# Kernel optimization log

Hardware: AMD Instinct MI355X
Metric: run time of the kernel (lower is better)

The kernel has to match this reference:

```python
import jax, jax.numpy as jnp
import numpy as np

B, H, S, D = 2, 8, 4096, 64
TEMPERATURE = 8.0


def setup_inputs() -> dict:
    key = jax.random.key(0)
    kq, kk, kv, km = jax.random.split(key, 4)
    q = jax.random.normal(kq, (B, H, S, D), dtype=jnp.float32)
    k = jax.random.normal(kk, (B, H, S, D), dtype=jnp.float32)
    v = jax.random.normal(kv, (B, H, S, D), dtype=jnp.float32)
    mask = jax.random.randint(km, (1, 1, S, S), 0, 2, dtype=jnp.int32)
    return {"q": q, "k": k, "v": v, "mask": mask}


def reference(q, k, v, mask):
    # scores = q @ k^T / temperature  -> [B,H,S,S]
    scores = jnp.einsum("bhqd,bhkd->bhqk", q, k) / TEMPERATURE
    # masked_fill(mask == 0, -inf)
    scores = jnp.where(mask == 0, -jnp.inf, scores)
    attn = jax.nn.softmax(scores, axis=-1)
    output = jnp.einsum("bhqk,bhkd->bhqd", attn, v)
    return (output, attn)
```

## Files before the change

### kernel.cpp

```cpp
#include <hip/hip_runtime.h>
#include <stdint.h>

typedef __attribute__((ext_vector_type(8))) short short8;
typedef __attribute__((ext_vector_type(4))) float float4v;

#define SEQ 4096
#define HD 64
#define QB 128
#define KT 64
#define HEADS 16
#define NT (SEQ / KT)
#define MWORDS (SEQ / 64)
#define TILE_BYTES 8192
#define QSCALE 0.18033688f

__device__ __forceinline__ ushort f2bf(float f) {
    union { float f; uint32_t u; } x; x.f = f;
    uint32_t u = x.u;
    return (ushort)((u + 0x7FFFu + ((u >> 16) & 1u)) >> 16);
}

__device__ __forceinline__ uint32_t cvt_pk_bf16(float lo, float hi) {
    uint32_t r;
    asm("v_cvt_pk_bf16_f32 %0, %1, %2" : "=v"(r) : "v"(lo), "v"(hi));
    return r;
}

__device__ __forceinline__ float exp2_hw(float x) { return __builtin_amdgcn_exp2f(x); }
__device__ __forceinline__ float log2_hw(float x) { return __builtin_amdgcn_logf(x); }

__device__ __forceinline__ void gload_lds16(const void* g, void* l) {
    __builtin_amdgcn_global_load_lds(
        (const __attribute__((address_space(1))) uint32_t*)g,
        (__attribute__((address_space(3))) uint32_t*)l, 16, 0, 0);
}

__global__ __launch_bounds__(256) void pack_mask_kernel(const int* __restrict__ mask,
                                                        unsigned long long* __restrict__ mb) {
    const int qrow = blockIdx.x;
    const int wave = threadIdx.x >> 6;
    const int lane = threadIdx.x & 63;
    const int* rp = mask + (size_t)qrow * SEQ;
    #pragma unroll
    for (int i = 0; i < 16; ++i) {
        const int widx = wave * 16 + i;
        const int mv = rp[widx * 64 + lane];
        unsigned long long b = __ballot(mv != 0);
        if (lane == 0) mb[(size_t)qrow * MWORDS + widx] = b;
    }
}

__global__ __launch_bounds__(256) void prep_kv_kernel(const float* __restrict__ kg,
                                                      const float* __restrict__ vg,
                                                      char* __restrict__ ktiles,
                                                      char* __restrict__ vtiles) {
    __shared__ __align__(16) float Tl[64][68];
    const int bid = blockIdx.x;
    const int tid = threadIdx.x;
    const float* Kg = kg + (size_t)bid * KT * HD;
    const float* Vg = vg + (size_t)bid * KT * HD;
    char* Kt = ktiles + (size_t)bid * TILE_BYTES;
    char* Vt = vtiles + (size_t)bid * TILE_BYTES;

    {
        const int r = tid >> 2, c0 = (tid & 3) * 16;
        #pragma unroll
        for (int j = 0; j < 4; ++j)
            *(float4v*)&Tl[r][c0 + j * 4] = *(const float4v*)(Kg + r * HD + c0 + j * 4);
    }
    __syncthreads();
    #pragma unroll
    for (int cc = 0; cc < 2; ++cc) {
        const int c = tid + cc * 256;
        const int t = c >> 7, h = (c >> 6) & 1, g = (c >> 4) & 3, li = c & 15;
        const int row = 32 * (t >> 1) + 8 * (li >> 2) + 4 * (t & 1) + (li & 3);
        const float* src = &Tl[row][h * 32 + g * 8];
        short8 w;
        #pragma unroll
        for (int e = 0; e < 8; ++e) w[e] = (short)f2bf(src[e]);
        *(short8*)(Kt + c * 16) = w;
    }
    __syncthreads();
    {
        const int r = tid >> 2, c0 = (tid & 3) * 16;
        #pragma unroll
        for (int j = 0; j < 4; ++j)
            *(float4v*)&Tl[r][c0 + j * 4] = *(const float4v*)(Vg + r * HD + c0 + j * 4);
    }
    __syncthreads();
    #pragma unroll
    for (int cc = 0; cc < 2; ++cc) {
        const int c = tid + cc * 256;
        const int dt = c >> 7, h = (c >> 6) & 1, g = (c >> 4) & 3, li = c & 15;
        short8 w;
        #pragma unroll
        for (int e = 0; e < 8; ++e) w[e] = (short)f2bf(Tl[h * 32 + g * 8 + e][dt * 16 + li]);
        *(short8*)(Vt + c * 16) = w;
    }
}

#define STAGE_K8(KTI, DST) do {                                                    \
    const char* _s = Ktile + (size_t)(KTI) * TILE_BYTES + wave * 1024 + lane * 16; \
    gload_lds16(_s, (char*)(DST) + wave * 1024);                                   \
} while (0)

#define STAGE2_K(KTI) do {                                                              \
    const char* _s = Ktile + (size_t)(KTI) * TILE_BYTES + ew * 2048 + lane * 16;        \
    char* _d = (char*)LdsK[(KTI) & 3] + ew * 2048;                                      \
    gload_lds16(_s, _d); gload_lds16(_s + 1024, _d + 1024);                             \
} while (0)

#define STAGE2_V(KTI) do {                                                              \
    const char* _s = Vtile + (size_t)(KTI) * TILE_BYTES + ew * 2048 + lane * 16;        \
    char* _d = (char*)LdsV[(KTI) & 3] + ew * 2048;                                      \
    gload_lds16(_s, _d); gload_lds16(_s + 1024, _d + 1024);                             \
} while (0)

__global__ __launch_bounds__(512, 4) void attn_kernel(
    const float* __restrict__ qg, const unsigned long long* __restrict__ mb,
    const char* __restrict__ ktiles, const char* __restrict__ vtiles,
    float* __restrict__ outg, float* __restrict__ attng)
{
    __shared__ __align__(16) char LdsK[4][TILE_BYTES];
    __shared__ __align__(16) char LdsV[4][TILE_BYTES];

    const int tid  = threadIdx.x;
    const int wave = tid >> 6;
    const int lane = tid & 63;
    const int g    = lane >> 4;
    const int li   = lane & 15;

    const int bid = blockIdx.x;
    const int blk = (bid & 7) * 64 + (bid >> 3);
    const int bh  = blk >> 5;
    const int qb  = blk & 31;

    const size_t qkvBase = (size_t)bh * SEQ * HD;
    const float* Qg = qg + qkvBase + (size_t)qb * QB * HD;
    const char* Ktile = ktiles + (size_t)bh * NT * TILE_BYTES;
    const char* Vtile = vtiles + (size_t)bh * NT * TILE_BYTES;

    const int wq0 = wave * 16;
    short8 aq[2];
    #pragma unroll
    for (int h = 0; h < 2; ++h) {
        const float* src = Qg + (wq0 + li) * HD + h * 32 + g * 8;
        short8 t;
        #pragma unroll
        for (int e = 0; e < 8; ++e) t[e] = (short)f2bf(src[e] * QSCALE);
        aq[h] = t;
    }

    const int qrow = qb * QB + wq0 + li;
    const unsigned long long* mrow = mb + (size_t)qrow * MWORDS;

    STAGE_K8(0, LdsK[0]);
    STAGE_K8(1, LdsK[1]);
    asm volatile("s_waitcnt vmcnt(1)" ::: "memory");
    __builtin_amdgcn_s_barrier();
    asm volatile("" ::: "memory");

    float lsum = 0.f;
    for (int kt = 0; kt < NT; ++kt) {
        if (kt + 2 < NT) STAGE_K8(kt + 2, LdsK[(kt + 2) % 3]);
        const unsigned long long mw = mrow[kt];
        const uint32_t mlo = (uint32_t)mw >> (g * 8);
        const uint32_t mhi = (uint32_t)(mw >> 32) >> (g * 8);

        const char* Kb = LdsK[kt % 3] + lane * 16;
        short8 bk[4][2];
        #pragma unroll
        for (int t = 0; t < 4; ++t)
            #pragma unroll
            for (int h = 0; h < 2; ++h)
                bk[t][h] = *(const short8*)(Kb + (t * 2 + h) * 1024);

        float4v accs[4];
        #pragma unroll
        for (int t = 0; t < 4; ++t) accs[t] = (float4v){0.f, 0.f, 0.f, 0.f};
        __builtin_amdgcn_s_setprio(1);
        #pragma unroll
        for (int t = 0; t < 4; ++t) {
            accs[t] = __builtin_amdgcn_mfma_f32_16x16x32_bf16(bk[t][0], aq[0], accs[t], 0, 0, 0);
            accs[t] = __builtin_amdgcn_mfma_f32_16x16x32_bf16(bk[t][1], aq[1], accs[t], 0, 0, 0);
        }
        __builtin_amdgcn_s_setprio(0);
        const uint32_t nib[4] = { mlo & 0xFu, (mlo >> 4) & 0xFu, mhi & 0xFu, (mhi >> 4) & 0xFu };
        #pragma unroll
        for (int t = 0; t < 4; ++t) {
            #pragma unroll
            for (int r = 0; r < 4; ++r) {
                const float e = exp2_hw(accs[t][r]);
                lsum += ((nib[t] >> r) & 1u) ? e : 0.f;
            }
        }
        if (kt < NT - 2) {
            asm volatile("s_waitcnt vmcnt(2)" ::: "memory");
            __builtin_amdgcn_s_barrier();
            asm volatile("" ::: "memory");
        } else if (kt == NT - 2) {
            asm volatile("s_waitcnt vmcnt(1)" ::: "memory");
            __builtin_amdgcn_s_barrier();
            asm volatile("" ::: "memory");
        }
    }
    lsum += __shfl_xor(lsum, 16);
    lsum += __shfl_xor(lsum, 32);
    const float linv2 = -log2_hw(lsum);

    float* attnT = attng + (size_t)bh * SEQ * SEQ + (size_t)qrow * SEQ + g * 8;
    float4v acco[4];
    #pragma unroll
    for (int dt = 0; dt < 4; ++dt) acco[dt] = (float4v){0.f, 0.f, 0.f, 0.f};

    const int odd = wave & 1;
    const int ew  = wave >> 1;

    __syncthreads();
    unsigned long long mwreg = mrow[0];
    if (!odd) {
        STAGE2_K(0); STAGE2_V(0);
        STAGE2_K(1); STAGE2_V(1);
        asm volatile("s_waitcnt vmcnt(0)" ::: "memory");
    }
    __builtin_amdgcn_s_barrier();
    asm volatile("" ::: "memory");

    float4v accs[4];
    for (int slot = 0; slot < 2 * NT + 1; ++slot) {
        const int half = slot & 1;
        int t_qk = -1, t_fin = -1;
        if (!odd) {
            if (!half) { const int t = slot >> 1; if (t < NT) t_qk = t; }
            else       t_fin = slot >> 1;
        } else {
            if (half)  t_qk = slot >> 1;
            else if (slot > 0) t_fin = (slot >> 1) - 1;
        }

        if (t_qk >= 0) {
            if (!odd && t_qk + 2 < NT) { STAGE2_K(t_qk + 2); STAGE2_V(t_qk + 2); }
            const char* Kb = LdsK[t_qk & 3] + lane * 16;
            short8 bk[4][2];
            #pragma unroll
            for (int t = 0; t < 4; ++t)
                #pragma unroll
                for (int h = 0; h < 2; ++h)
                    bk[t][h] = *(const short8*)(Kb + (t * 2 + h) * 1024);
            #pragma unroll
            for (int t = 0; t < 4; ++t) accs[t] = (float4v){0.f, 0.f, 0.f, 0.f};
            __builtin_amdgcn_s_setprio(1);
            #pragma unroll
            for (int t = 0; t < 4; ++t) {
                accs[t] = __builtin_amdgcn_mfma_f32_16x16x32_bf16(bk[t][0], aq[0], accs[t], 0, 0, 0);
                accs[t] = __builtin_amdgcn_mfma_f32_16x16x32_bf16(bk[t][1], aq[1], accs[t], 0, 0, 0);
            }
            __builtin_amdgcn_s_setprio(0);
        }

        if (t_fin >= 0) {
            const char* Vb = LdsV[t_fin & 3] + lane * 16;
            short8 vb[4][2];
            #pragma unroll
            for (int t = 0; t < 4; ++t)
                #pragma unroll
                for (int h = 0; h < 2; ++h)
                    vb[t][h] = *(const short8*)(Vb + (t * 2 + h) * 1024);

            const uint32_t mlo = (uint32_t)mwreg >> (g * 8);
            const uint32_t mhi = (uint32_t)(mwreg >> 32) >> (g * 8);
            const uint32_t nib[4] = { mlo & 0xFu, (mlo >> 4) & 0xFu, mhi & 0xFu, (mhi >> 4) & 0xFu };
            float4v pv[4];
            #pragma unroll
            for (int t = 0; t < 4; ++t)
                #pragma unroll
                for (int r = 0; r < 4; ++r) {
                    const float e = exp2_hw(accs[t][r] + linv2);
                    pv[t][r] = ((nib[t] >> r) & 1u) ? e : 0.f;
                }

            float* ap = attnT + t_fin * KT;
            *(float4v*)(ap)      = pv[0];
            *(float4v*)(ap + 4)  = pv[1];
            *(float4v*)(ap + 32) = pv[2];
            *(float4v*)(ap + 36) = pv[3];

            if (t_fin + 1 < NT) mwreg = mrow[t_fin + 1];

            uint32_t pk[4][2];
            #pragma unroll
            for (int t = 0; t < 4; ++t) {
                pk[t][0] = cvt_pk_bf16(pv[t][0], pv[t][1]);
                pk[t][1] = cvt_pk_bf16(pv[t][2], pv[t][3]);
            }
            union { uint32_t u[4]; short8 s; } pa0, pa1;
            pa0.u[0] = pk[0][0]; pa0.u[1] = pk[0][1]; pa0.u[2] = pk[1][0]; pa0.u[3] = pk[1][1];
            pa1.u[0] = pk[2][0]; pa1.u[1] = pk[2][1]; pa1.u[2] = pk[3][0]; pa1.u[3] = pk[3][1];

            __builtin_amdgcn_s_setprio(1);
            #pragma unroll
            for (int dt = 0; dt < 4; ++dt) {
                acco[dt] = __builtin_amdgcn_mfma_f32_16x16x32_bf16(vb[dt][0], pa0.s, acco[dt], 0, 0, 0);
                acco[dt] = __builtin_amdgcn_mfma_f32_16x16x32_bf16(vb[dt][1], pa1.s, acco[dt], 0, 0, 0);
            }
            __builtin_amdgcn_s_setprio(0);
        }

        if (slot < 2 * NT) {
            if (t_qk >= 0 || t_fin >= 0)
                asm volatile("s_waitcnt vmcnt(5)" ::: "memory");
            __builtin_amdgcn_s_barrier();
            asm volatile("" ::: "memory");
        }
    }

    float* outW = outg + qkvBase + (size_t)qrow * HD + g * 4;
    #pragma unroll
    for (int dt = 0; dt < 4; ++dt) {
        *(float4v*)(outW + dt * 16) = acco[dt];
    }
}

extern "C" void kernel_launch(void* const* d_in, const int* in_sizes, int n_in,
                              void* d_out, int out_size, void* d_ws, size_t ws_size,
                              hipStream_t stream) {
    (void)in_sizes; (void)n_in; (void)out_size; (void)ws_size;
    const float* q = (const float*)d_in[0];
    const float* k = (const float*)d_in[1];
    const float* v = (const float*)d_in[2];
    const int* mask = (const int*)d_in[3];

    float* outp  = (float*)d_out;
    float* attnp = outp + (size_t)2 * 8 * SEQ * HD;

    char* ws = (char*)d_ws;
    unsigned long long* mb = (unsigned long long*)ws;
    char* ktiles = ws + (size_t)2 * 1024 * 1024;
    char* vtiles = ws + (size_t)10 * 1024 * 1024;

    pack_mask_kernel<<<SEQ, 256, 0, stream>>>(mask, mb);
    prep_kv_kernel<<<HEADS * NT, 256, 0, stream>>>(k, v, ktiles, vtiles);
    attn_kernel<<<HEADS * (SEQ / QB), 512, 0, stream>>>(q, mb, ktiles, vtiles, outp, attnp);
}
```

Before: 383.3 us.

## Split pass-1 row-sum over key halves, each wave computing two query blocks

Pass 1 (softmax denominator) now divides the key range in two: waves 0-3 handle the first half of key tiles and waves 4-7 the second, each wave covering 32 query rows so every K tile loaded from LDS feeds two MFMA row blocks. Partial sums are combined through LDS before the second pass. The aim is to halve LDS K reads per MFMA and raise MFMA density in the first pass. The cost is extra Q registers, a second mask load per tile, and an LDS reduction with a full barrier.

```diff
diff --git a/kernel.cpp b/kernel.cpp
--- a/kernel.cpp
+++ b/kernel.cpp
@@ -10,6 +10,7 @@
 #define KT 64
 #define HEADS 16
 #define NT (SEQ / KT)
+#define NTH (NT / 2)
 #define MWORDS (SEQ / 64)
 #define TILE_BYTES 8192
 #define QSCALE 0.18033688f
@@ -99,11 +100,6 @@
     }
 }
 
-#define STAGE_K8(KTI, DST) do {                                                    \
-    const char* _s = Ktile + (size_t)(KTI) * TILE_BYTES + wave * 1024 + lane * 16; \
-    gload_lds16(_s, (char*)(DST) + wave * 1024);                                   \
-} while (0)
-
 #define STAGE2_K(KTI) do {                                                              \
     const char* _s = Ktile + (size_t)(KTI) * TILE_BYTES + ew * 2048 + lane * 16;        \
     char* _d = (char*)LdsK[(KTI) & 3] + ew * 2048;                                      \
@@ -113,6 +109,17 @@
 #define STAGE2_V(KTI) do {                                                              \
     const char* _s = Vtile + (size_t)(KTI) * TILE_BYTES + ew * 2048 + lane * 16;        \
     char* _d = (char*)LdsV[(KTI) & 3] + ew * 2048;                                      \
+} while (0)
+#undef STAGE2_V
+#define STAGE2_V(KTI) do {                                                              \
+    const char* _s = Vtile + (size_t)(KTI) * TILE_BYTES + ew * 2048 + lane * 16;        \
+    char* _d = (char*)LdsV[(KTI) & 3] + ew * 2048;                                      \
+    gload_lds16(_s, _d); gload_lds16(_s + 1024, _d + 1024);                             \
+} while (0)
+
+#define STAGE_P1(TI, DST) do {                                                          \
+    const char* _s = Ktile + (size_t)(kt0 + (TI)) * TILE_BYTES + w4 * 2048 + lane * 16; \
+    char* _d = (char*)(DST) + w4 * 2048;                                                \
     gload_lds16(_s, _d); gload_lds16(_s + 1024, _d + 1024);                             \
 } while (0)
 
@@ -154,59 +161,98 @@
     const int qrow = qb * QB + wq0 + li;
     const unsigned long long* mrow = mb + (size_t)qrow * MWORDS;
 
-    STAGE_K8(0, LdsK[0]);
-    STAGE_K8(1, LdsK[1]);
-    asm volatile("s_waitcnt vmcnt(1)" ::: "memory");
+    const int half = wave >> 2;
+    const int w4   = wave & 3;
+    const int kt0  = half * NTH;
+
+    short8 aq1[2][2];
+    #pragma unroll
+    for (int u = 0; u < 2; ++u)
+        #pragma unroll
+        for (int h = 0; h < 2; ++h) {
+            const float* src = Qg + (w4 * 32 + u * 16 + li) * HD + h * 32 + g * 8;
+            short8 t;
+            #pragma unroll
+            for (int e = 0; e < 8; ++e) t[e] = (short)f2bf(src[e] * QSCALE);
+            aq1[u][h] = t;
+        }
+    const unsigned long long* m1[2] = {
+        mb + (size_t)(qb * QB + w4 * 32 + li) * MWORDS,
+        mb + (size_t)(qb * QB + w4 * 32 + 16 + li) * MWORDS
+    };
+    char* buf0 = half ? LdsV[0] : LdsK[0];
+    char* buf1 = half ? LdsV[1] : LdsK[1];
+    char* buf2 = half ? LdsV[2] : LdsK[2];
+    char* bufs[3] = { buf0, buf1, buf2 };
+
+    STAGE_P1(0, buf0);
+    STAGE_P1(1, buf1);
+    asm volatile("s_waitcnt vmcnt(2)" ::: "memory");
     __builtin_amdgcn_s_barrier();
     asm volatile("" ::: "memory");
 
-    float lsum = 0.f;
-    for (int kt = 0; kt < NT; ++kt) {
-        if (kt + 2 < NT) STAGE_K8(kt + 2, LdsK[(kt + 2) % 3]);
-        const unsigned long long mw = mrow[kt];
-        const uint32_t mlo = (uint32_t)mw >> (g * 8);
-        const uint32_t mhi = (uint32_t)(mw >> 32) >> (g * 8);
-
-        const char* Kb = LdsK[kt % 3] + lane * 16;
+    float lsum[2] = {0.f, 0.f};
+    for (int t = 0; t < NTH; ++t) {
+        if (t + 2 < NTH) STAGE_P1(t + 2, bufs[(t + 2) % 3]);
+        const unsigned long long mw0 = m1[0][kt0 + t];
+        const unsigned long long mw1 = m1[1][kt0 + t];
+
+        const char* Kb = bufs[t % 3] + lane * 16;
         short8 bk[4][2];
         #pragma unroll
-        for (int t = 0; t < 4; ++t)
+        for (int tt = 0; tt < 4; ++tt)
             #pragma unroll
             for (int h = 0; h < 2; ++h)
-                bk[t][h] = *(const short8*)(Kb + (t * 2 + h) * 1024);
-
-        float4v accs[4];
-        #pragma unroll
-        for (int t = 0; t < 4; ++t) accs[t] = (float4v){0.f, 0.f, 0.f, 0.f};
-        __builtin_amdgcn_s_setprio(1);
-        #pragma unroll
-        for (int t = 0; t < 4; ++t) {
-            accs[t] = __builtin_amdgcn_mfma_f32_16x16x32_bf16(bk[t][0], aq[0], accs[t], 0, 0, 0);
-            accs[t] = __builtin_amdgcn_mfma_f32_16x16x32_bf16(bk[t][1], aq[1], accs[t], 0, 0, 0);
-        }
-        __builtin_amdgcn_s_setprio(0);
-        const uint32_t nib[4] = { mlo & 0xFu, (mlo >> 4) & 0xFu, mhi & 0xFu, (mhi >> 4) & 0xFu };
-        #pragma unroll
-        for (int t = 0; t < 4; ++t) {
-            #pragma unroll
-            for (int r = 0; r < 4; ++r) {
-                const float e = exp2_hw(accs[t][r]);
-                lsum += ((nib[t] >> r) & 1u) ? e : 0.f;
+                bk[tt][h] = *(const short8*)(Kb + (tt * 2 + h) * 1024);
+
+        #pragma unroll
+        for (int u = 0; u < 2; ++u) {
+            const unsigned long long mw = (u == 0) ? mw0 : mw1;
+            float4v accs[4];
+            #pragma unroll
+            for (int tt = 0; tt < 4; ++tt) accs[tt] = (float4v){0.f, 0.f, 0.f, 0.f};
+            __builtin_amdgcn_s_setprio(1);
+            #pragma unroll
+            for (int tt = 0; tt < 4; ++tt) {
+                accs[tt] = __builtin_amdgcn_mfma_f32_16x16x32_bf16(bk[tt][0], aq1[u][0], accs[tt], 0, 0, 0);
+                accs[tt] = __builtin_amdgcn_mfma_f32_16x16x32_bf16(bk[tt][1], aq1[u][1], accs[tt], 0, 0, 0);
             }
-        }
-        if (kt < NT - 2) {
+            __builtin_amdgcn_s_setprio(0);
+            const uint32_t mlo = (uint32_t)mw >> (g * 8);
+            const uint32_t mhi = (uint32_t)(mw >> 32) >> (g * 8);
+            const uint32_t nib[4] = { mlo & 0xFu, (mlo >> 4) & 0xFu, mhi & 0xFu, (mhi >> 4) & 0xFu };
+            float ls = 0.f;
+            #pragma unroll
+            for (int tt = 0; tt < 4; ++tt)
+                #pragma unroll
+                for (int r = 0; r < 4; ++r) {
+                    const float e = exp2_hw(accs[tt][r]);
+                    ls += ((nib[tt] >> r) & 1u) ? e : 0.f;
+                }
+            lsum[u] += ls;
+        }
+
+        if (t < NTH - 2) {
             asm volatile("s_waitcnt vmcnt(2)" ::: "memory");
             __builtin_amdgcn_s_barrier();
             asm volatile("" ::: "memory");
-        } else if (kt == NT - 2) {
-            asm volatile("s_waitcnt vmcnt(1)" ::: "memory");
+        } else if (t == NTH - 2) {
+            asm volatile("s_waitcnt vmcnt(0)" ::: "memory");
             __builtin_amdgcn_s_barrier();
             asm volatile("" ::: "memory");
         }
     }
-    lsum += __shfl_xor(lsum, 16);
-    lsum += __shfl_xor(lsum, 32);
-    const float linv2 = -log2_hw(lsum);
+
+    float* lsumLds = (float*)LdsK[3];
+    #pragma unroll
+    for (int u = 0; u < 2; ++u) {
+        float s = lsum[u];
+        s += __shfl_xor(s, 16);
+        s += __shfl_xor(s, 32);
+        if (g == 0) lsumLds[half * 128 + w4 * 32 + u * 16 + li] = s;
+    }
+    __syncthreads();
+    const float linv2 = -log2_hw(lsumLds[wq0 + li] + lsumLds[128 + wq0 + li]);
 
     float* attnT = attng + (size_t)bh * SEQ * SEQ + (size_t)qrow * SEQ + g * 8;
     float4v acco[4];
@@ -216,7 +262,6 @@
     const int odd = wave & 1;
     const int ew  = wave >> 1;
 
-    __syncthreads();
     unsigned long long mwreg = mrow[0];
     if (!odd) {
         STAGE2_K(0); STAGE2_V(0);
@@ -228,13 +273,13 @@
 
     float4v accs[4];
     for (int slot = 0; slot < 2 * NT + 1; ++slot) {
-        const int half = slot & 1;
+        const int shalf = slot & 1;
         int t_qk = -1, t_fin = -1;
         if (!odd) {
-            if (!half) { const int t = slot >> 1; if (t < NT) t_qk = t; }
-            else       t_fin = slot >> 1;
+            if (!shalf) { const int t = slot >> 1; if (t < NT) t_qk = t; }
+            else        t_fin = slot >> 1;
         } else {
-            if (half)  t_qk = slot >> 1;
+            if (shalf)  t_qk = slot >> 1;
             else if (slot > 0) t_fin = (slot >> 1) - 1;
         }
 
```

Result: no change. 389.6 us (+1.6%).

## Ping-pong the row-sum pass: staggered MFMA and exp phases across wave pairs

Applied to the files above, without the earlier changes.

The first pass, which computes softmax row sums, is restructured to match the second pass's ping-pong schedule. Even and odd waves alternate between the QK MFMA phase and the exp/mask-accumulate phase in staggered slots. Only even waves now issue K staging, using a 4-deep LDS ring. This aims to overlap matrix-core work with transcendental VALU work across waves, at the cost of twice as many barrier slots and more intricate vmcnt bookkeeping.

```diff
diff --git a/kernel.cpp b/kernel.cpp
--- a/kernel.cpp
+++ b/kernel.cpp
@@ -99,11 +99,6 @@
     }
 }
 
-#define STAGE_K8(KTI, DST) do {                                                    \
-    const char* _s = Ktile + (size_t)(KTI) * TILE_BYTES + wave * 1024 + lane * 16; \
-    gload_lds16(_s, (char*)(DST) + wave * 1024);                                   \
-} while (0)
-
 #define STAGE2_K(KTI) do {                                                              \
     const char* _s = Ktile + (size_t)(KTI) * TILE_BYTES + ew * 2048 + lane * 16;        \
     char* _d = (char*)LdsK[(KTI) & 3] + ew * 2048;                                      \
@@ -154,52 +149,76 @@
     const int qrow = qb * QB + wq0 + li;
     const unsigned long long* mrow = mb + (size_t)qrow * MWORDS;
 
-    STAGE_K8(0, LdsK[0]);
-    STAGE_K8(1, LdsK[1]);
-    asm volatile("s_waitcnt vmcnt(1)" ::: "memory");
+    const int odd = wave & 1;
+    const int ew  = wave >> 1;
+
+    float lsum = 0.f;
+    unsigned long long mwreg = mrow[0];
+    __builtin_amdgcn_sched_barrier(0);
+    if (!odd) {
+        STAGE2_K(0); STAGE2_K(1);
+        asm volatile("s_waitcnt vmcnt(0)" ::: "memory");
+    }
     __builtin_amdgcn_s_barrier();
     asm volatile("" ::: "memory");
 
-    float lsum = 0.f;
-    for (int kt = 0; kt < NT; ++kt) {
-        if (kt + 2 < NT) STAGE_K8(kt + 2, LdsK[(kt + 2) % 3]);
-        const unsigned long long mw = mrow[kt];
-        const uint32_t mlo = (uint32_t)mw >> (g * 8);
-        const uint32_t mhi = (uint32_t)(mw >> 32) >> (g * 8);
-
-        const char* Kb = LdsK[kt % 3] + lane * 16;
-        short8 bk[4][2];
-        #pragma unroll
-        for (int t = 0; t < 4; ++t)
-            #pragma unroll
-            for (int h = 0; h < 2; ++h)
-                bk[t][h] = *(const short8*)(Kb + (t * 2 + h) * 1024);
-
-        float4v accs[4];
-        #pragma unroll
-        for (int t = 0; t < 4; ++t) accs[t] = (float4v){0.f, 0.f, 0.f, 0.f};
-        __builtin_amdgcn_s_setprio(1);
-        #pragma unroll
-        for (int t = 0; t < 4; ++t) {
-            accs[t] = __builtin_amdgcn_mfma_f32_16x16x32_bf16(bk[t][0], aq[0], accs[t], 0, 0, 0);
-            accs[t] = __builtin_amdgcn_mfma_f32_16x16x32_bf16(bk[t][1], aq[1], accs[t], 0, 0, 0);
-        }
-        __builtin_amdgcn_s_setprio(0);
-        const uint32_t nib[4] = { mlo & 0xFu, (mlo >> 4) & 0xFu, mhi & 0xFu, (mhi >> 4) & 0xFu };
-        #pragma unroll
-        for (int t = 0; t < 4; ++t) {
-            #pragma unroll
-            for (int r = 0; r < 4; ++r) {
-                const float e = exp2_hw(accs[t][r]);
-                lsum += ((nib[t] >> r) & 1u) ? e : 0.f;
-            }
-        }
-        if (kt < NT - 2) {
-            asm volatile("s_waitcnt vmcnt(2)" ::: "memory");
-            __builtin_amdgcn_s_barrier();
-            asm volatile("" ::: "memory");
-        } else if (kt == NT - 2) {
-            asm volatile("s_waitcnt vmcnt(1)" ::: "memory");
+    float4v accs[4];
+    for (int slot = 0; slot < 2 * NT + 1; ++slot) {
+        const int shalf = slot & 1;
+        int t_qk = -1, t_ex = -1;
+        if (!odd) {
+            if (!shalf) { const int t = slot >> 1; if (t < NT) t_qk = t; }
+            else        t_ex = slot >> 1;
+        } else {
+            if (shalf)  t_qk = slot >> 1;
+            else if (slot > 0) t_ex = (slot >> 1) - 1;
+        }
+
+        if (t_qk >= 0) {
+            if (!odd && t_qk + 2 < NT) STAGE2_K(t_qk + 2);
+            const char* Kb = LdsK[t_qk & 3] + lane * 16;
+            short8 bk[4][2];
+            #pragma unroll
+            for (int t = 0; t < 4; ++t)
+                #pragma unroll
+                for (int h = 0; h < 2; ++h)
+                    bk[t][h] = *(const short8*)(Kb + (t * 2 + h) * 1024);
+            #pragma unroll
+            for (int t = 0; t < 4; ++t) accs[t] = (float4v){0.f, 0.f, 0.f, 0.f};
+            __builtin_amdgcn_s_setprio(1);
+            #pragma unroll
+            for (int t = 0; t < 4; ++t) {
+                accs[t] = __builtin_amdgcn_mfma_f32_16x16x32_bf16(bk[t][0], aq[0], accs[t], 0, 0, 0);
+                accs[t] = __builtin_amdgcn_mfma_f32_16x16x32_bf16(bk[t][1], aq[1], accs[t], 0, 0, 0);
+            }
+            __builtin_amdgcn_s_setprio(0);
+        }
+
+        if (t_ex >= 0) {
+            const uint32_t mlo = (uint32_t)mwreg >> (g * 8);
+            const uint32_t mhi = (uint32_t)(mwreg >> 32) >> (g * 8);
+            const uint32_t nib[4] = { mlo & 0xFu, (mlo >> 4) & 0xFu, mhi & 0xFu, (mhi >> 4) & 0xFu };
+            #pragma unroll
+            for (int t = 0; t < 4; ++t)
+                #pragma unroll
+                for (int r = 0; r < 4; ++r) {
+                    const float e = exp2_hw(accs[t][r]);
+                    lsum += ((nib[t] >> r) & 1u) ? e : 0.f;
+                }
+            if (t_ex + 1 < NT) mwreg = mrow[t_ex + 1];
+        }
+
+        if (slot < 2 * NT) {
+            if (!odd) {
+                if (t_qk >= 0 && t_qk + 2 < NT)
+                    asm volatile("s_waitcnt vmcnt(2)" ::: "memory");
+                else if (t_qk >= 0)
+                    asm volatile("s_waitcnt vmcnt(1)" ::: "memory");
+                else
+                    asm volatile("s_waitcnt vmcnt(2)" ::: "memory");
+            } else {
+                asm volatile("s_waitcnt vmcnt(1)" ::: "memory");
+            }
             __builtin_amdgcn_s_barrier();
             asm volatile("" ::: "memory");
         }
@@ -213,11 +232,8 @@
     #pragma unroll
     for (int dt = 0; dt < 4; ++dt) acco[dt] = (float4v){0.f, 0.f, 0.f, 0.f};
 
-    const int odd = wave & 1;
-    const int ew  = wave >> 1;
-
     __syncthreads();
-    unsigned long long mwreg = mrow[0];
+    mwreg = mrow[0];
     if (!odd) {
         STAGE2_K(0); STAGE2_V(0);
         STAGE2_K(1); STAGE2_V(1);
@@ -226,15 +242,14 @@
     __builtin_amdgcn_s_barrier();
     asm volatile("" ::: "memory");
 
-    float4v accs[4];
     for (int slot = 0; slot < 2 * NT + 1; ++slot) {
-        const int half = slot & 1;
+        const int shalf = slot & 1;
         int t_qk = -1, t_fin = -1;
         if (!odd) {
-            if (!half) { const int t = slot >> 1; if (t < NT) t_qk = t; }
-            else       t_fin = slot >> 1;
+            if (!shalf) { const int t = slot >> 1; if (t < NT) t_qk = t; }
+            else        t_fin = slot >> 1;
         } else {
-            if (half)  t_qk = slot >> 1;
+            if (shalf)  t_qk = slot >> 1;
             else if (slot > 0) t_fin = (slot >> 1) - 1;
         }
 
```

Measured after the change: 403.6 us. 1.05x slower.
